# Kernel optimization log

Measured on AMD Instinct MI355X. Metric: run time of the kernel, lower is better.

## Reference

```python
import jax, jax.numpy as jnp
import numpy as np

MASK_THRED = 1        # init kwarg mask_thred
TRIPLE_WEIGHT = 1.0   # init kwarg triple_weight (scales gradient of shifted branch)
NEG = -1e30
EPS = 1e-8


def setup_inputs() -> dict:
    key = jax.random.key(0)
    k1, k2 = jax.random.split(key)
    x = jax.random.normal(k1, (2, 128, 96, 96), dtype=jnp.float32)
    mask = jax.random.randint(k2, (96, 96), 0, 2, dtype=jnp.int32)
    return {"x": x, "mask": mask}


def reference(x, mask):
    # x: (B, C, H, W); former = x[:, :C//2], latter = x[:, C//2:]
    B, C, H, W = x.shape
    c2 = C // 2
    hw = H * W

    # shift_sz=1, stride=1, mask_thred=1 -> a location is 'masked' iff mask >= 1
    flag = mask.reshape(hw) >= MASK_THRED  # (hw,) True = inside hole

    former, latter = x[:, :c2], x[:, c2:]

    # similarity path is non-differentiable in the original (hard argmax, detached latter)
    lat = jax.lax.stop_gradient(latter).reshape(B, c2, hw).transpose(0, 2, 1)  # (B, hw, c2)
    # original normalizes only the candidate (non-masked) patches (NCC filters)
    lat_n = lat / jnp.maximum(jnp.linalg.norm(lat, axis=-1, keepdims=True), EPS)

    # cross-correlation of every location against every (normalized) candidate
    sim = jnp.einsum('bic,bjc->bij', lat, lat_n)  # (B, hw, hw)
    # only non-masked locations are valid candidates j
    sim = jnp.where(flag[None, None, :], NEG, sim)
    idx = jnp.argmax(sim, axis=-1)  # (B, hw) nearest non-masked neighbor per location

    # shift: copy the FORMER feature from the matched non-masked location
    fmr = former.reshape(B, c2, hw).transpose(0, 2, 1)  # (B, hw, c2)
    gathered = jnp.take_along_axis(fmr, idx[:, :, None], axis=1)  # (B, hw, c2)

    # triple_weight scales only the gradient of the shifted branch (fwd unchanged)
    tw = jnp.float32(TRIPLE_WEIGHT)
    gathered = gathered * tw + jax.lax.stop_gradient(gathered * (1.0 - tw))

    # shifted features only at masked locations, zero elsewhere
    shift = jnp.where(flag[None, :, None], gathered, jnp.float32(0.0))
    shift = shift.transpose(0, 2, 1).reshape(B, c2, H, W)

    # triple: (former, latter, shifted) -> (B, 3*C//2, H, W)
    return jnp.concatenate([former, latter, shift], axis=1)
```

## Files before the change

kernel.cpp:

```cpp
#include <hip/hip_runtime.h>
#include <math.h>

#define HW 9216
#define C2 64
#define NSTRIP 288
#define NCH 16
#define EPSN 1e-8f

typedef _Float16 f16x8  __attribute__((ext_vector_type(8)));
typedef float    f32x16 __attribute__((ext_vector_type(16)));

__global__ void compact_kernel(const int* __restrict__ mask, int* __restrict__ ilist,
                               int* __restrict__ jlist, int* __restrict__ slotmap,
                               int* __restrict__ counts) {
    int t = threadIdx.x;
    int base = t * 9;
    unsigned fl = 0; int cnt = 0;
#pragma unroll
    for (int k = 0; k < 9; k++) {
        int f = (mask[base + k] >= 1) ? 1 : 0;
        fl |= (unsigned)f << k;
        cnt += f;
    }
    int lane = t & 63, wave = t >> 6;
    int v = cnt;
#pragma unroll
    for (int off = 1; off < 64; off <<= 1) {
        int u = __shfl_up(v, off, 64);
        if (lane >= off) v += u;
    }
    __shared__ int wsum[16];
    if (lane == 63) wsum[wave] = v;
    __syncthreads();
    int woff = 0;
#pragma unroll
    for (int w = 0; w < 16; w++) if (w < wave) woff += wsum[w];
    int incl = v + woff;
    int excl = incl - cnt;
    int posF = excl, posU = base - excl;
#pragma unroll
    for (int k = 0; k < 9; k++) {
        int p = base + k;
        if ((fl >> k) & 1u) { slotmap[p] = posF | 0x80000000; ilist[posF++] = p; }
        else               { slotmap[p] = posU;              jlist[posU++] = p; }
    }
    if (t == 1023) { counts[0] = incl; counts[1] = HW - incl; }
}

__global__ void norm_kernel(const float* __restrict__ x, float* __restrict__ invAll) {
    int t = blockIdx.x * 256 + threadIdx.x;
    int cc = t & 7;
    int pb = t >> 3;
    int b = pb / HW, p = pb - b * HW;
    const float* xl = x + (size_t)(b * 128 + 64) * HW + p;
    float ss = 0.f;
#pragma unroll
    for (int e = 0; e < 8; e++) { float w = xl[(size_t)(cc * 8 + e) * HW]; ss = fmaf(w, w, ss); }
    ss += __shfl_xor(ss, 1, 64);
    ss += __shfl_xor(ss, 2, 64);
    ss += __shfl_xor(ss, 4, 64);
    if (cc == 0) invAll[pb] = 1.0f / fmaxf(sqrtf(ss), EPSN);
}

__global__ void pack_kernel(const float* __restrict__ x, const int* __restrict__ slotmap,
                            const float* __restrict__ invAll,
                            _Float16* __restrict__ aH, _Float16* __restrict__ aL,
                            _Float16* __restrict__ bH, _Float16* __restrict__ bL,
                            unsigned long long* __restrict__ amax) {
    int p = blockIdx.x * 256 + threadIdx.x;
    int cc = blockIdx.y;
    int b = blockIdx.z;
    if (cc == 0) amax[(size_t)b * HW + p] = 0ull;
    int sm = slotmap[p];
    int flagged = (sm >> 31) & 1;
    int slot = sm & 0x7fffffff;
    const float* xl = x + (size_t)(b * 128 + 64) * HW + p;
    float scale = flagged ? 1.0f : invAll[b * HW + p];
    f16x8 hh, ll;
#pragma unroll
    for (int e = 0; e < 8; e++) {
        float w = xl[(size_t)(cc * 8 + e) * HW] * scale;
        _Float16 h = (_Float16)w;
        hh[e] = h;
        ll[e] = (_Float16)((w - (float)h) * 2048.0f);
    }
    int ks = cc >> 1, g = cc & 1;
    int strip = slot >> 5, ln = slot & 31;
    size_t off = ((((size_t)b * NSTRIP + strip) * 4 + ks) * 64 + (g * 32 + ln)) * 8;
    _Float16* dh = flagged ? aH : bH;
    _Float16* dl = flagged ? aL : bL;
    *(f16x8*)(dh + off) = hh;
    *(f16x8*)(dl + off) = ll;
}

__device__ __forceinline__ unsigned int ordf(float f) {
    unsigned int u = __float_as_uint(f);
    return (u & 0x80000000u) ? ~u : (u | 0x80000000u);
}

__global__ __launch_bounds__(256, 2) void argmax_kernel(
    const _Float16* __restrict__ aH, const _Float16* __restrict__ aL,
    const _Float16* __restrict__ bH, const _Float16* __restrict__ bL,
    const int* __restrict__ ilist, const int* __restrict__ counts,
    unsigned long long* __restrict__ amax)
{
    int ni = counts[0];
    if (blockIdx.x * 256 >= ni) return;
    int nj = counts[1];
    int b = blockIdx.z, s = blockIdx.y;
    int wave = threadIdx.x >> 6, l = threadIdx.x & 63;
    int base = (blockIdx.x * 4 + wave) * 64;
    if (base >= ni) return;
    int g = l >> 5, ln = l & 31;
    int strip0 = base >> 5;

    const f16x8* apH = (const f16x8*)aH + ((size_t)b * NSTRIP + strip0) * 256 + l;
    const f16x8* apL = (const f16x8*)aL + ((size_t)b * NSTRIP + strip0) * 256 + l;
    f16x8 xh0 = apH[0],   xh1 = apH[64],  xh2 = apH[128], xh3 = apH[192];
    f16x8 xl0 = apL[0],   xl1 = apL[64],  xl2 = apL[128], xl3 = apL[192];
    f16x8 yh0 = apH[256], yh1 = apH[320], yh2 = apH[384], yh3 = apH[448];
    f16x8 yl0 = apL[256], yl1 = apL[320], yl2 = apL[384], yl3 = apL[448];

    int njt = (nj + 31) >> 5;
    int tpc = (njt + NCH - 1) / NCH;
    int jt0 = s * tpc, jt1 = min(jt0 + tpc, njt);
    float bv0 = -INFINITY, bv1 = -INFINITY;
    int bj0 = -1, bj1 = -1;
    const f16x8* bpH0 = (const f16x8*)bH + (size_t)b * NSTRIP * 256 + l;
    const f16x8* bpL0 = (const f16x8*)bL + (size_t)b * NSTRIP * 256 + l;

    for (int jt = jt0; jt < jt1; ++jt) {
        const f16x8* bpH = bpH0 + (size_t)jt * 256;
        const f16x8* bpL = bpL0 + (size_t)jt * 256;
        f16x8 bh0 = bpH[0], bh1 = bpH[64], bh2 = bpH[128], bh3 = bpH[192];
        f16x8 bl0 = bpL[0], bl1 = bpL[64], bl2 = bpL[128], bl3 = bpL[192];
        f32x16 cH0 = {}, cC0 = {}, cH1 = {}, cC1 = {};
        cH0 = __builtin_amdgcn_mfma_f32_32x32x16_f16(bh0, xh0, cH0, 0, 0, 0);
        cC0 = __builtin_amdgcn_mfma_f32_32x32x16_f16(bh0, xl0, cC0, 0, 0, 0);
        cC0 = __builtin_amdgcn_mfma_f32_32x32x16_f16(bl0, xh0, cC0, 0, 0, 0);
        cH0 = __builtin_amdgcn_mfma_f32_32x32x16_f16(bh1, xh1, cH0, 0, 0, 0);
        cC0 = __builtin_amdgcn_mfma_f32_32x32x16_f16(bh1, xl1, cC0, 0, 0, 0);
        cC0 = __builtin_amdgcn_mfma_f32_32x32x16_f16(bl1, xh1, cC0, 0, 0, 0);
        cH0 = __builtin_amdgcn_mfma_f32_32x32x16_f16(bh2, xh2, cH0, 0, 0, 0);
        cC0 = __builtin_amdgcn_mfma_f32_32x32x16_f16(bh2, xl2, cC0, 0, 0, 0);
        cC0 = __builtin_amdgcn_mfma_f32_32x32x16_f16(bl2, xh2, cC0, 0, 0, 0);
        cH0 = __builtin_amdgcn_mfma_f32_32x32x16_f16(bh3, xh3, cH0, 0, 0, 0);
        cC0 = __builtin_amdgcn_mfma_f32_32x32x16_f16(bh3, xl3, cC0, 0, 0, 0);
        cC0 = __builtin_amdgcn_mfma_f32_32x32x16_f16(bl3, xh3, cC0, 0, 0, 0);
        cH1 = __builtin_amdgcn_mfma_f32_32x32x16_f16(bh0, yh0, cH1, 0, 0, 0);
        cC1 = __builtin_amdgcn_mfma_f32_32x32x16_f16(bh0, yl0, cC1, 0, 0, 0);
        cC1 = __builtin_amdgcn_mfma_f32_32x32x16_f16(bl0, yh0, cC1, 0, 0, 0);
        cH1 = __builtin_amdgcn_mfma_f32_32x32x16_f16(bh1, yh1, cH1, 0, 0, 0);
        cC1 = __builtin_amdgcn_mfma_f32_32x32x16_f16(bh1, yl1, cC1, 0, 0, 0);
        cC1 = __builtin_amdgcn_mfma_f32_32x32x16_f16(bl1, yh1, cC1, 0, 0, 0);
        cH1 = __builtin_amdgcn_mfma_f32_32x32x16_f16(bh2, yh2, cH1, 0, 0, 0);
        cC1 = __builtin_amdgcn_mfma_f32_32x32x16_f16(bh2, yl2, cC1, 0, 0, 0);
        cC1 = __builtin_amdgcn_mfma_f32_32x32x16_f16(bl2, yh2, cC1, 0, 0, 0);
        cH1 = __builtin_amdgcn_mfma_f32_32x32x16_f16(bh3, yh3, cH1, 0, 0, 0);
        cC1 = __builtin_amdgcn_mfma_f32_32x32x16_f16(bh3, yl3, cC1, 0, 0, 0);
        cC1 = __builtin_amdgcn_mfma_f32_32x32x16_f16(bl3, yh3, cC1, 0, 0, 0);
        int jb = jt << 5;
#pragma unroll
        for (int r = 0; r < 16; ++r) {
            int row = (r & 3) + 8 * (r >> 2) + 4 * g;
            int j = jb + row;
            float v0 = fmaf(cC0[r], 4.8828125e-4f , cH0[r]);
            float v1 = fmaf(cC1[r], 4.8828125e-4f, cH1[r]);
            if (j < nj && v0 > bv0) { bv0 = v0; bj0 = j; }
            if (j < nj && v1 > bv1) { bv1 = v1; bj1 = j; }
        }
    }
    unsigned long long k0 = ((unsigned long long)ordf(bv0) << 32) |
                            (unsigned long long)(~(unsigned int)bj0);
    unsigned long long k1 = ((unsigned long long)ordf(bv1) << 32) |
                            (unsigned long long)(~(unsigned int)bj1);
    unsigned long long o0 = __shfl_xor(k0, 32, 64);
    unsigned long long o1 = __shfl_xor(k1, 32, 64);
    if (o0 > k0) k0 = o0;
    if (o1 > k1) k1 = o1;
    int il0 = base + ln, il1 = base + 32 + ln;
    if (g == 0) {
        if (il0 < ni && (unsigned)(k0 >> 32) > 0x007FFFFFu)
            atomicMax(&amax[(size_t)b * HW + ilist[il0]], k0);
        if (il1 < ni && (unsigned)(k1 >> 32) > 0x007FFFFFu)
            atomicMax(&amax[(size_t)b * HW + ilist[il1]], k1);
    }
}

__global__ void epilogue_kernel(const float4* __restrict__ x4, const float* __restrict__ x,
                                const int* __restrict__ mask,
                                const unsigned long long* __restrict__ amax,
                                const int* __restrict__ jlist, float4* __restrict__ out4) {
    const int q = HW / 4;
    int t = blockIdx.x * blockDim.x + threadIdx.x;
    if (t >= 2 * 192 * q) return;
    int pos4 = t % q;
    int c = (t / q) % 192;
    int b = t / (192 * q);
    if (c < 128) {
        out4[t] = x4[((size_t)b * 128 + c) * q + pos4];
    } else {
        float4 v = make_float4(0.f, 0.f, 0.f, 0.f);
        float* vp = &v.x;
        int pos = pos4 * 4;
        const float* xf = x + (size_t)(b * 128 + (c - 128)) * HW;
#pragma unroll
        for (int k = 0; k < 4; k++) {
            int p = pos + k;
            if (mask[p] >= 1) {
                unsigned long long key = amax[(size_t)b * HW + p];
                int j = 0;
                if (key != 0ull) j = jlist[(int)(~(unsigned int)key)];
                vp[k] = xf[j];
            }
        }
        out4[t] = v;
    }
}

extern "C" void kernel_launch(void* const* d_in, const int* in_sizes, int n_in,
                              void* d_out, int out_size, void* d_ws, size_t ws_size,
                              hipStream_t stream) {
    const float* x = (const float*)d_in[0];
    const int* mask = (const int*)d_in[1];
    float4* out4 = (float4*)d_out;

    char* ws = (char*)d_ws;
    int*   counts  = (int*)ws;
    int*   ilist   = (int*)(ws + 128);
    int*   jlist   = (int*)(ws + 36992);
    int*   slotmap = (int*)(ws + 73856);
    unsigned long long* amax = (unsigned long long*)(ws + 110720);
    float* invAll  = (float*)(ws + 258176);
    _Float16* aH = (_Float16*)(ws + 331904);
    _Float16* aL = (_Float16*)(ws + 331904 + 1 * 2359296);
    _Float16* bH = (_Float16*)(ws + 331904 + 2 * 2359296);
    _Float16* bL = (_Float16*)(ws + 331904 + 3 * 2359296);

    compact_kernel<<<1, 1024, 0, stream>>>(mask, ilist, jlist, slotmap, counts);
    norm_kernel<<<(2 * HW * 8) / 256, 256, 0, stream>>>(x, invAll);
    {
        dim3 grid(HW / 256, 8, 2);
        pack_kernel<<<grid, 256, 0, stream>>>(x, slotmap, invAll, aH, aL, bH, bL, amax);
    }
    {
        dim3 grid(NSTRIP / 8, NCH, 2);
        argmax_kernel<<<grid, 256, 0, stream>>>(aH, aL, bH, bL, ilist, counts, amax);
    }
    {
        int n = 2 * 192 * (HW / 4);
        epilogue_kernel<<<(n + 255) / 256, 256, 0, stream>>>((const float4*)x, x, mask,
                                                             amax, jlist, out4);
    }
}
```

Before: 109.1 us.

## Share candidate tiles through double-buffered LDS and merge prep kernels

Each argmax block now loads the candidate B tiles cooperatively into a double-buffered LDS array, with each wave fetching two of eight fragments and prefetching the next tile while computing. Previously all four waves loaded the same B tiles independently from global memory. The compaction and norm kernels are fused into a single prep launch that also zeros amax, removing one launch. Per-tile __syncthreads barriers are added, and the early exit for waves with base >= ni is removed, so some waves may do redundant work.

```diff
diff --git a/kernel.cpp b/kernel.cpp
--- a/kernel.cpp
+++ b/kernel.cpp
@@ -10,67 +10,69 @@
 typedef _Float16 f16x8  __attribute__((ext_vector_type(8)));
 typedef float    f32x16 __attribute__((ext_vector_type(16)));
 
-__global__ void compact_kernel(const int* __restrict__ mask, int* __restrict__ ilist,
-                               int* __restrict__ jlist, int* __restrict__ slotmap,
-                               int* __restrict__ counts) {
-    int t = threadIdx.x;
-    int base = t * 9;
-    unsigned fl = 0; int cnt = 0;
-#pragma unroll
-    for (int k = 0; k < 9; k++) {
-        int f = (mask[base + k] >= 1) ? 1 : 0;
-        fl |= (unsigned)f << k;
-        cnt += f;
-    }
-    int lane = t & 63, wave = t >> 6;
-    int v = cnt;
-#pragma unroll
-    for (int off = 1; off < 64; off <<= 1) {
-        int u = __shfl_up(v, off, 64);
-        if (lane >= off) v += u;
-    }
-    __shared__ int wsum[16];
-    if (lane == 63) wsum[wave] = v;
-    __syncthreads();
-    int woff = 0;
-#pragma unroll
-    for (int w = 0; w < 16; w++) if (w < wave) woff += wsum[w];
-    int incl = v + woff;
-    int excl = incl - cnt;
-    int posF = excl, posU = base - excl;
-#pragma unroll
-    for (int k = 0; k < 9; k++) {
-        int p = base + k;
-        if ((fl >> k) & 1u) { slotmap[p] = posF | 0x80000000; ilist[posF++] = p; }
-        else               { slotmap[p] = posU;              jlist[posU++] = p; }
-    }
-    if (t == 1023) { counts[0] = incl; counts[1] = HW - incl; }
-}
-
-__global__ void norm_kernel(const float* __restrict__ x, float* __restrict__ invAll) {
-    int t = blockIdx.x * 256 + threadIdx.x;
-    int cc = t & 7;
-    int pb = t >> 3;
-    int b = pb / HW, p = pb - b * HW;
-    const float* xl = x + (size_t)(b * 128 + 64) * HW + p;
-    float ss = 0.f;
-#pragma unroll
-    for (int e = 0; e < 8; e++) { float w = xl[(size_t)(cc * 8 + e) * HW]; ss = fmaf(w, w, ss); }
-    ss += __shfl_xor(ss, 1, 64);
-    ss += __shfl_xor(ss, 2, 64);
-    ss += __shfl_xor(ss, 4, 64);
-    if (cc == 0) invAll[pb] = 1.0f / fmaxf(sqrtf(ss), EPSN);
+__global__ void prep_kernel(const float* __restrict__ x, const int* __restrict__ mask,
+                            int* __restrict__ ilist, int* __restrict__ jlist,
+                            int* __restrict__ slotmap, int* __restrict__ counts,
+                            float* __restrict__ invAll, unsigned long long* __restrict__ amax) {
+    if (blockIdx.x < 576) {
+        int t = blockIdx.x * 256 + threadIdx.x;
+        int cc = t & 7;
+        int pb = t >> 3;
+        int b = pb / HW, p = pb - b * HW;
+        const float* xl = x + (size_t)(b * 128 + 64) * HW + p;
+        float ss = 0.f;
+#pragma unroll
+        for (int e = 0; e < 8; e++) { float w = xl[(size_t)(cc * 8 + e) * HW]; ss = fmaf(w, w, ss); }
+        ss += __shfl_xor(ss, 1, 64);
+        ss += __shfl_xor(ss, 2, 64);
+        ss += __shfl_xor(ss, 4, 64);
+        if (cc == 0) {
+            invAll[pb] = 1.0f / fmaxf(sqrtf(ss), EPSN);
+            amax[pb] = 0ull;
+        }
+    } else {
+        int t = threadIdx.x;
+        int base = t * 36;
+        unsigned long long fl = 0ull; int cnt = 0;
+#pragma unroll
+        for (int k = 0; k < 36; k++) {
+            int f = (mask[base + k] >= 1) ? 1 : 0;
+            fl |= (unsigned long long)f << k;
+            cnt += f;
+        }
+        int lane = t & 63, wave = t >> 6;
+        int v = cnt;
+#pragma unroll
+        for (int off = 1; off < 64; off <<= 1) {
+            int u = __shfl_up(v, off, 64);
+            if (lane >= off) v += u;
+        }
+        __shared__ int wsum[4];
+        if (lane == 63) wsum[wave] = v;
+        __syncthreads();
+        int woff = 0;
+#pragma unroll
+        for (int w = 0; w < 4; w++) if (w < wave) woff += wsum[w];
+        int incl = v + woff;
+        int excl = incl - cnt;
+        int posF = excl, posU = base - excl;
+#pragma unroll
+        for (int k = 0; k < 36; k++) {
+            int p = base + k;
+            if ((fl >> k) & 1ull) { slotmap[p] = posF | 0x80000000; ilist[posF++] = p; }
+            else                  { slotmap[p] = posU;              jlist[posU++] = p; }
+        }
+        if (t == 255) { counts[0] = incl; counts[1] = HW - incl; }
+    }
 }
 
 __global__ void pack_kernel(const float* __restrict__ x, const int* __restrict__ slotmap,
                             const float* __restrict__ invAll,
                             _Float16* __restrict__ aH, _Float16* __restrict__ aL,
-                            _Float16* __restrict__ bH, _Float16* __restrict__ bL,
-                            unsigned long long* __restrict__ amax) {
+                            _Float16* __restrict__ bH, _Float16* __restrict__ bL) {
     int p = blockIdx.x * 256 + threadIdx.x;
     int cc = blockIdx.y;
     int b = blockIdx.z;
-    if (cc == 0) amax[(size_t)b * HW + p] = 0ull;
     int sm = slotmap[p];
     int flagged = (sm >> 31) & 1;
     int slot = sm & 0x7fffffff;
@@ -107,12 +109,18 @@
     int ni = counts[0];
     if (blockIdx.x * 256 >= ni) return;
     int nj = counts[1];
-    int b = blockIdx.z, s = blockIdx.y;
+    int njt = (nj + 31) >> 5;
+    int tpc = (njt + NCH - 1) / NCH;
+    int s = blockIdx.y;
+    int jt0 = s * tpc, jt1 = min(jt0 + tpc, njt);
+    if (jt0 >= jt1) return;
+    int b = blockIdx.z;
     int wave = threadIdx.x >> 6, l = threadIdx.x & 63;
     int base = (blockIdx.x * 4 + wave) * 64;
-    if (base >= ni) return;
     int g = l >> 5, ln = l & 31;
     int strip0 = base >> 5;
+
+    __shared__ f16x8 lds[2][8][64];
 
     const f16x8* apH = (const f16x8*)aH + ((size_t)b * NSTRIP + strip0) * 256 + l;
     const f16x8* apL = (const f16x8*)aL + ((size_t)b * NSTRIP + strip0) * 256 + l;
@@ -121,19 +129,35 @@
     f16x8 yh0 = apH[256], yh1 = apH[320], yh2 = apH[384], yh3 = apH[448];
     f16x8 yl0 = apL[256], yl1 = apL[320], yl2 = apL[384], yl3 = apL[448];
 
-    int njt = (nj + 31) >> 5;
-    int tpc = (njt + NCH - 1) / NCH;
-    int jt0 = s * tpc, jt1 = min(jt0 + tpc, njt);
+    int f0 = wave * 2;
+    const f16x8* s0 = (const f16x8*)((f0 < 4) ? bH : bL) +
+                      (size_t)b * NSTRIP * 256 + (size_t)(f0 & 3) * 64 + l;
+    const f16x8* s1 = (const f16x8*)((f0 + 1 < 4) ? bH : bL) +
+                      (size_t)b * NSTRIP * 256 + (size_t)((f0 + 1) & 3) * 64 + l;
+
+    {
+        f16x8 t0 = s0[(size_t)jt0 * 256];
+        f16x8 t1 = s1[(size_t)jt0 * 256];
+        lds[0][f0][l] = t0;
+        lds[0][f0 + 1][l] = t1;
+    }
+    __syncthreads();
+
     float bv0 = -INFINITY, bv1 = -INFINITY;
     int bj0 = -1, bj1 = -1;
-    const f16x8* bpH0 = (const f16x8*)bH + (size_t)b * NSTRIP * 256 + l;
-    const f16x8* bpL0 = (const f16x8*)bL + (size_t)b * NSTRIP * 256 + l;
-
-    for (int jt = jt0; jt < jt1; ++jt) {
-        const f16x8* bpH = bpH0 + (size_t)jt * 256;
-        const f16x8* bpL = bpL0 + (size_t)jt * 256;
-        f16x8 bh0 = bpH[0], bh1 = bpH[64], bh2 = bpH[128], bh3 = bpH[192];
-        f16x8 bl0 = bpL[0], bl1 = bpL[64], bl2 = bpL[128], bl3 = bpL[192];
+    int cur = 0;
+
+    for (int jt = jt0; jt < jt1; ++jt, cur ^= 1) {
+        f16x8 n0, n1;
+        bool more = (jt + 1 < jt1);
+        if (more) {
+            n0 = s0[(size_t)(jt + 1) * 256];
+            n1 = s1[(size_t)(jt + 1) * 256];
+        }
+        f16x8 bh0 = lds[cur][0][l], bh1 = lds[cur][1][l];
+        f16x8 bh2 = lds[cur][2][l], bh3 = lds[cur][3][l];
+        f16x8 bl0 = lds[cur][4][l], bl1 = lds[cur][5][l];
+        f16x8 bl2 = lds[cur][6][l], bl3 = lds[cur][7][l];
         f32x16 cH0 = {}, cC0 = {}, cH1 = {}, cC1 = {};
         cH0 = __builtin_amdgcn_mfma_f32_32x32x16_f16(bh0, xh0, cH0, 0, 0, 0);
         cC0 = __builtin_amdgcn_mfma_f32_32x32x16_f16(bh0, xl0, cC0, 0, 0, 0);
@@ -169,7 +193,13 @@
             if (j < nj && v0 > bv0) { bv0 = v0; bj0 = j; }
             if (j < nj && v1 > bv1) { bv1 = v1; bj1 = j; }
         }
-    }
+        if (more) {
+            lds[cur ^ 1][f0][l] = n0;
+            lds[cur ^ 1][f0 + 1][l] = n1;
+        }
+        __syncthreads();
+    }
+
     unsigned long long k0 = ((unsigned long long)ordf(bv0) << 32) |
                             (unsigned long long)(~(unsigned int)bj0);
     unsigned long long k1 = ((unsigned long long)ordf(bv1) << 32) |
@@ -237,11 +267,11 @@
     _Float16* bH = (_Float16*)(ws + 331904 + 2 * 2359296);
     _Float16* bL = (_Float16*)(ws + 331904 + 3 * 2359296);
 
-    compact_kernel<<<1, 1024, 0, stream>>>(mask, ilist, jlist, slotmap, counts);
-    norm_kernel<<<(2 * HW * 8) / 256, 256, 0, stream>>>(x, invAll);
+    prep_kernel<<<577, 256, 0, stream>>>(x, mask, ilist, jlist, slotmap, counts,
+                                         invAll, amax);
     {
         dim3 grid(HW / 256, 8, 2);
-        pack_kernel<<<grid, 256, 0, stream>>>(x, slotmap, invAll, aH, aL, bH, bL, amax);
+        pack_kernel<<<grid, 256, 0, stream>>>(x, slotmap, invAll, aH, aL, bH, bL);
     }
     {
         dim3 grid(NSTRIP / 8, NCH, 2);
```

Measured after the change: 109.7 us. Within noise of the previous version (+0.6%).
